# Kernel optimization log

Measured on AMD Instinct MI355X. Metric: run time of the kernel, lower is better.

Reference implementation:

```python
import jax, jax.numpy as jnp
import numpy as np

DIM = 1024
HEADS = 16
DIM_HEAD = 64
INNER = HEADS * DIM_HEAD
EPS = 1e-6


def elu_feature_map(t):
    # F.elu(x) + 1
    return jnp.where(t > 0, t + 1.0, jnp.exp(t))


def setup_inputs() -> dict:
    key = jax.random.key(0)
    k1, k2, k3, k4 = jax.random.split(key, 4)
    B, N = 4, 8192
    x = jax.random.normal(k1, (B, N, DIM), dtype=jnp.float32)
    s_in = 1.0 / np.sqrt(DIM)
    s_out = 1.0 / np.sqrt(INNER)
    Wqkv = jax.random.uniform(k2, (DIM, 3 * INNER), dtype=jnp.float32, minval=-s_in, maxval=s_in)
    Wout = jax.random.uniform(k3, (INNER, DIM), dtype=jnp.float32, minval=-s_out, maxval=s_out)
    bout = jax.random.uniform(k4, (DIM,), dtype=jnp.float32, minval=-s_out, maxval=s_out)
    return {"x": x, "Wqkv": Wqkv, "Wout": Wout, "bout": bout}


def reference(x, Wqkv, Wout, bout):
    B, N, D = x.shape
    qkv = x @ Wqkv  # [B,N,3*INNER]
    q, k, v = jnp.split(qkv, 3, axis=-1)
    # b n (h d) -> b h n d
    resh = lambda t: t.reshape(B, N, HEADS, DIM_HEAD).transpose(0, 2, 1, 3)
    q, k, v = resh(q), resh(k), resh(v)
    q = elu_feature_map(q)
    k = elu_feature_map(k)
    kv = jnp.einsum('bhnd,bhnf->bhdf', k, v)          # [B,H,d,d]
    k_sum = k.sum(axis=-2)                             # [B,H,d]
    qkv_out = jnp.einsum('bhnd,bhdf->bhnf', q, kv)    # [B,H,N,d]
    q_k_sum = jnp.einsum('bhnd,bhd->bhn', q, k_sum)   # [B,H,N]
    out = qkv_out / (q_k_sum[..., None] + EPS)
    out = out.transpose(0, 2, 1, 3).reshape(B, N, INNER)  # b h n d -> b n (h d)
    return out @ Wout + bout
```

## Files before the change

### kernel.cpp

```cpp
#include <hip/hip_runtime.h>
#include <hip/hip_bf16.h>
#include <math.h>


typedef unsigned short ushort_t;
typedef __attribute__((ext_vector_type(8))) short s8v;
typedef __attribute__((ext_vector_type(4))) float f32x4;

#define MFMA(a,b,c) __builtin_amdgcn_mfma_f32_16x16x32_bf16((a),(b),(c),0,0,0)

typedef __attribute__((address_space(3))) unsigned int as3_u32;
typedef __attribute__((address_space(1))) const unsigned int as1_u32c;

__device__ __forceinline__ void g2l16(const void* g, void* l) {
    __builtin_amdgcn_global_load_lds((as1_u32c*)g, (as3_u32*)l, 16, 0, 0);
}

__device__ __forceinline__ float bf2f(ushort_t u) {
    union { float f; unsigned v; } x; x.v = ((unsigned)u) << 16; return x.f;
}
__device__ __forceinline__ ushort_t f2bf(float f) {
    union { float f; unsigned v; } x; x.f = f;
    unsigned r = x.v + 0x7fffu + ((x.v >> 16) & 1u);
    return (ushort_t)(r >> 16);
}
__device__ __forceinline__ float elu1(float t) { return t > 0.0f ? t + 1.0f : expf(t); }

__global__ void k_cast(const float* __restrict__ in, ushort_t* __restrict__ out, int n8) {
    int i = blockIdx.x * blockDim.x + threadIdx.x;
    if (i >= n8) return;
    const float4* p = (const float4*)in;
    float4 a = p[(size_t)i * 2], b = p[(size_t)i * 2 + 1];
    uint4 o;
    o.x = (unsigned)f2bf(a.x) | ((unsigned)f2bf(a.y) << 16);
    o.y = (unsigned)f2bf(a.z) | ((unsigned)f2bf(a.w) << 16);
    o.z = (unsigned)f2bf(b.x) | ((unsigned)f2bf(b.y) << 16);
    o.w = (unsigned)f2bf(b.z) | ((unsigned)f2bf(b.w) << 16);
    *(uint4*)(out + (size_t)i * 8) = o;
}

__global__ __launch_bounds__(256) void k_transpose(const float* __restrict__ W,
                                                   ushort_t* __restrict__ WT, int K, int N) {
    __shared__ float s[32][33];
    const int t = threadIdx.x;
    const int k0 = blockIdx.x * 32, n0 = blockIdx.y * 32;
    const int kr = t >> 3, n4 = (t & 7) * 4;
    float4 v = *(const float4*)(W + (size_t)(k0 + kr) * N + n0 + n4);
    s[kr][n4 + 0] = v.x; s[kr][n4 + 1] = v.y; s[kr][n4 + 2] = v.z; s[kr][n4 + 3] = v.w;
    __syncthreads();
    const int nr = kr, k4 = n4;
    unsigned lo = (unsigned)f2bf(s[k4 + 0][nr]) | ((unsigned)f2bf(s[k4 + 1][nr]) << 16);
    unsigned hi = (unsigned)f2bf(s[k4 + 2][nr]) | ((unsigned)f2bf(s[k4 + 3][nr]) << 16);
    *(uint2*)(WT + (size_t)(n0 + nr) * K + k0 + k4) = make_uint2(lo, hi);
}

template<int MODE>
__global__ __launch_bounds__(512, 1) void k_gemm(
    const ushort_t* __restrict__ A, const ushort_t* __restrict__ B,
    ushort_t* __restrict__ obf, const float* __restrict__ bout, float* __restrict__ of)
{
    constexpr int PLANE = 256 * 32;
    constexpr int BUFS  = 4 * PLANE;
    __shared__ ushort_t lds[2 * BUFS];

    const int t = threadIdx.x, l = t & 63, w = t >> 6;
    const int wr = w >> 2, wc = w & 3;
    const size_t m0 = (size_t)blockIdx.x * 256;
    const size_t n0 = (size_t)blockIdx.y * 256;

    f32x4 acc[8][4];
    const f32x4 z = {0.f, 0.f, 0.f, 0.f};
#pragma unroll
    for (int i = 0; i < 8; i++)
#pragma unroll
        for (int j = 0; j < 4; j++) acc[i][j] = z;

    const int swz = (((l & 3) ^ ((l >> 3) & 3)) << 3);
    const ushort_t* gAl = A + (m0 + (size_t)(w * 16) + (l >> 2)) * 1024 + swz;
    const ushort_t* gBl = B + (n0 + (size_t)(w * 16) + (l >> 2)) * 1024 + swz;
    const int dRow = (w * 16) * 32;

    const int la15 = l & 15;
    const int sA = (((l >> 4) ^ ((la15 >> 1) & 3)) << 3);

    g2l16(gAl,               &lds[0 * PLANE + dRow]);
    g2l16(gAl + 128 * 1024,  &lds[0 * PLANE + 128 * 32 + dRow]);
    g2l16(gBl,               &lds[1 * PLANE + dRow]);
    g2l16(gBl + 128 * 1024,  &lds[1 * PLANE + 128 * 32 + dRow]);
    g2l16(gAl + 32,              &lds[2 * PLANE + dRow]);
    g2l16(gAl + 128 * 1024 + 32, &lds[2 * PLANE + 128 * 32 + dRow]);
    g2l16(gBl + 32,              &lds[3 * PLANE + dRow]);
    g2l16(gBl + 128 * 1024 + 32, &lds[3 * PLANE + 128 * 32 + dRow]);

    for (int T = 0; T < 16; ++T) {
        const int base  = (T & 1) * BUFS;
        const int nbase = BUFS - base;
        const size_t kT1 = (size_t)(T + 1) * 64;
        s8v af[8], bf[4];

        asm volatile("s_waitcnt vmcnt(4)" ::: "memory");
        __builtin_amdgcn_sched_barrier(0);
        __builtin_amdgcn_s_barrier();
        __builtin_amdgcn_sched_barrier(0);
        if (T < 15) {
            g2l16(gAl + kT1,              &lds[nbase + 0 * PLANE + dRow]);
            g2l16(gAl + 128 * 1024 + kT1, &lds[nbase + 0 * PLANE + 128 * 32 + dRow]);
            g2l16(gBl + kT1,              &lds[nbase + 1 * PLANE + dRow]);
            g2l16(gBl + 128 * 1024 + kT1, &lds[nbase + 1 * PLANE + 128 * 32 + dRow]);
        }
#pragma unroll
        for (int nf = 0; nf < 4; nf++)
            bf[nf] = *(const s8v*)&lds[base + 1 * PLANE + (wc * 64 + nf * 16 + la15) * 32 + sA];
#pragma unroll
        for (int mf = 0; mf < 8; mf++)
            af[mf] = *(const s8v*)&lds[base + 0 * PLANE + (wr * 128 + mf * 16 + la15) * 32 + sA];
        __builtin_amdgcn_s_setprio(1);
#pragma unroll
        for (int mf = 0; mf < 8; mf++)
#pragma unroll
            for (int nf = 0; nf < 4; nf++)
                acc[mf][nf] = MFMA(af[mf], bf[nf], acc[mf][nf]);
        __builtin_amdgcn_s_setprio(0);

        if (T < 15) asm volatile("s_waitcnt vmcnt(4)" ::: "memory");
        else        asm volatile("s_waitcnt vmcnt(0)" ::: "memory");
        __builtin_amdgcn_sched_barrier(0);
        __builtin_amdgcn_s_barrier();
        __builtin_amdgcn_sched_barrier(0);
        if (T < 15) {
            g2l16(gAl + 32 + kT1,              &lds[nbase + 2 * PLANE + dRow]);
            g2l16(gAl + 128 * 1024 + 32 + kT1, &lds[nbase + 2 * PLANE + 128 * 32 + dRow]);
            g2l16(gBl + 32 + kT1,              &lds[nbase + 3 * PLANE + dRow]);
            g2l16(gBl + 128 * 1024 + 32 + kT1, &lds[nbase + 3 * PLANE + 128 * 32 + dRow]);
        }
#pragma unroll
        for (int nf = 0; nf < 4; nf++)
            bf[nf] = *(const s8v*)&lds[base + 3 * PLANE + (wc * 64 + nf * 16 + la15) * 32 + sA];
#pragma unroll
        for (int mf = 0; mf < 8; mf++)
            af[mf] = *(const s8v*)&lds[base + 2 * PLANE + (wr * 128 + mf * 16 + la15) * 32 + sA];
        __builtin_amdgcn_s_setprio(1);
#pragma unroll
        for (int mf = 0; mf < 8; mf++)
#pragma unroll
            for (int nf = 0; nf < 4; nf++)
                acc[mf][nf] = MFMA(af[mf], bf[nf], acc[mf][nf]);
        __builtin_amdgcn_s_setprio(0);
    }

    const int r4 = (l >> 4) * 4;
    if (MODE == 0) {
#pragma unroll
        for (int mf = 0; mf < 8; mf++)
#pragma unroll
            for (int nf = 0; nf < 4; nf++) {
                const size_t colb = n0 + wc * 64 + nf * 16;
                const bool feat = colb < 2048;
#pragma unroll
                for (int r = 0; r < 4; r++) {
                    const size_t row = m0 + wr * 128 + mf * 16 + r4 + r;
                    float v = acc[mf][nf][r];
                    obf[row * 3072 + colb + la15] = f2bf(feat ? elu1(v) : v);
                }
            }
    } else {
#pragma unroll
        for (int mf = 0; mf < 8; mf++)
#pragma unroll
            for (int nf = 0; nf < 4; nf++) {
                const size_t col = n0 + wc * 64 + nf * 16 + la15;
                const float bo = bout[col];
#pragma unroll
                for (int r = 0; r < 4; r++) {
                    const size_t row = m0 + wr * 128 + mf * 16 + r4 + r;
                    of[row * 1024 + col] = acc[mf][nf][r] + bo;
                }
            }
    }
}

#define KST 136
__global__ __launch_bounds__(256) void k_kv(
    const ushort_t* __restrict__ qkv, float* __restrict__ kv, float* __restrict__ ksum)
{
    __shared__ ushort_t kT[64 * KST];
    __shared__ ushort_t vT[64 * KST];
    __shared__ float ksl[64];
    const int t = threadIdx.x, l = t & 63, w = t >> 6;
    const int wr = w >> 1, wc = w & 1;
    const int h = blockIdx.x;
    const int b = blockIdx.z;
    const ushort_t* qkvb = qkv + (size_t)b * 8192 * 3072;
    float* kvh = kv + ((size_t)b * 16 + h) * 4096;
    float* ksh = ksum + (size_t)b * 1024 + h * 64;
    const int n00 = blockIdx.y * 512;
    const f32x4 z = {0.f, 0.f, 0.f, 0.f};
    f32x4 acc[2][2] = {{z, z}, {z, z}};
    float ksloc[4] = {0.f, 0.f, 0.f, 0.f};
    const int sd0 = (t & 15) * 4;
    if (t < 64) ksl[t] = 0.f;

    for (int c = 0; c < 4; c++) {
        __syncthreads();
        const int n0 = n00 + c * 128;
#pragma unroll
        for (int i = 0; i < 8; i++) {
            int n = i * 16 + (t >> 4);
            const ushort_t* kp = qkvb + (size_t)(n0 + n) * 3072 + 1024 + h * 64 + sd0;
            ushort4 kw = *(const ushort4*)kp;
            ushort4 vw = *(const ushort4*)(kp + 1024);
            ksloc[0] += bf2f(kw.x); ksloc[1] += bf2f(kw.y);
            ksloc[2] += bf2f(kw.z); ksloc[3] += bf2f(kw.w);
            kT[(sd0 + 0) * KST + n] = kw.x; kT[(sd0 + 1) * KST + n] = kw.y;
            kT[(sd0 + 2) * KST + n] = kw.z; kT[(sd0 + 3) * KST + n] = kw.w;
            vT[(sd0 + 0) * KST + n] = vw.x; vT[(sd0 + 1) * KST + n] = vw.y;
            vT[(sd0 + 2) * KST + n] = vw.z; vT[(sd0 + 3) * KST + n] = vw.w;
        }
        __syncthreads();
#pragma unroll
        for (int kb = 0; kb < 128; kb += 32) {
            s8v af[2], bfr[2];
#pragma unroll
            for (int ma = 0; ma < 2; ma++) {
                int d = wr * 32 + ma * 16 + (l & 15);
                af[ma] = *(const s8v*)&kT[d * KST + kb + (l >> 4) * 8];
            }
#pragma unroll
            for (int fb = 0; fb < 2; fb++) {
                int f = wc * 32 + fb * 16 + (l & 15);
                bfr[fb] = *(const s8v*)&vT[f * KST + kb + (l >> 4) * 8];
            }
#pragma unroll
            for (int ma = 0; ma < 2; ma++)
#pragma unroll
                for (int fb = 0; fb < 2; fb++)
                    acc[ma][fb] = MFMA(af[ma], bfr[fb], acc[ma][fb]);
        }
    }
    atomicAdd(&ksl[sd0 + 0], ksloc[0]); atomicAdd(&ksl[sd0 + 1], ksloc[1]);
    atomicAdd(&ksl[sd0 + 2], ksloc[2]); atomicAdd(&ksl[sd0 + 3], ksloc[3]);
    __syncthreads();
    if (t < 64) atomicAdd(&ksh[t], ksl[t]);
#pragma unroll
    for (int ma = 0; ma < 2; ma++)
#pragma unroll
        for (int fb = 0; fb < 2; fb++)
#pragma unroll
            for (int r = 0; r < 4; r++) {
                int d = wr * 32 + ma * 16 + (l >> 4) * 4 + r;
                int f = wc * 32 + fb * 16 + (l & 15);
                atomicAdd(&kvh[f * 64 + d], acc[ma][fb][r]);
            }
}

#define AST 72
__global__ __launch_bounds__(256) void k_apply(
    const ushort_t* __restrict__ qkv, const float* __restrict__ kv,
    const float* __restrict__ ksum, ushort_t* __restrict__ attn)
{
    __shared__ ushort_t kvb[64 * AST];
    const int t = threadIdx.x, l = t & 63, w = t >> 6;
    const int la15 = l & 15;
    const int row0 = blockIdx.x * 32;
    const int b = row0 >> 13;
    const f32x4 z = {0.f, 0.f, 0.f, 0.f};

    for (int hh = 0; hh < 8; hh++) {
        const int h = blockIdx.y * 8 + hh;
        const float* kvh = kv + ((size_t)b * 16 + h) * 4096;
        const float* ksh = ksum + (size_t)b * 1024 + h * 64;
        __syncthreads();
        {
            const int f = t >> 2, d0 = (t & 3) * 16;
            const float* src = kvh + f * 64 + d0;
            s8v v0, v1;
#pragma unroll
            for (int j = 0; j < 8; j++) {
                v0[j] = (short)f2bf(src[j]);
                v1[j] = (short)f2bf(src[j + 8]);
            }
            *(s8v*)&kvb[f * AST + d0]     = v0;
            *(s8v*)&kvb[f * AST + d0 + 8] = v1;
        }
        __syncthreads();
        float ksv[16];
        {
            const float* kp = ksh + (l >> 4) * 8;
            *(float4*)&ksv[0]  = *(const float4*)(kp);
            *(float4*)&ksv[4]  = *(const float4*)(kp + 4);
            *(float4*)&ksv[8]  = *(const float4*)(kp + 32);
            *(float4*)&ksv[12] = *(const float4*)(kp + 36);
        }
        f32x4 acc[2] = {z, z};
        float pd[2] = {0.f, 0.f};
#pragma unroll
        for (int ks = 0; ks < 2; ks++) {
            const int f = w * 16 + la15;
            s8v bfr = *(const s8v*)&kvb[f * AST + ks * 32 + (l >> 4) * 8];
#pragma unroll
            for (int ma = 0; ma < 2; ma++) {
                int row = row0 + ma * 16 + la15;
                s8v afr = *(const s8v*)(qkv + (size_t)row * 3072 + h * 64 + ks * 32 + (l >> 4) * 8);
#pragma unroll
                for (int j = 0; j < 8; j++)
                    pd[ma] += bf2f((ushort_t)afr[j]) * ksv[ks * 8 + j];
                acc[ma] = MFMA(afr, bfr, acc[ma]);
            }
        }
#pragma unroll
        for (int ma = 0; ma < 2; ma++) {
            pd[ma] += __shfl_xor(pd[ma], 16, 64);
            pd[ma] += __shfl_xor(pd[ma], 32, 64);
        }
#pragma unroll
        for (int ma = 0; ma < 2; ma++)
#pragma unroll
            for (int r = 0; r < 4; r++) {
                int lrow = (l >> 4) * 4 + r;
                float dot = __shfl(pd[ma], lrow, 64);
                float dv = 1.f / (dot + 1e-6f);
                int row = row0 + ma * 16 + lrow;
                int f = w * 16 + la15;
                attn[(size_t)row * 1024 + h * 64 + f] = f2bf(acc[ma][r] * dv);
            }
    }
}

extern "C" void kernel_launch(void* const* d_in, const int* in_sizes, int n_in,
                              void* d_out, int out_size, void* d_ws, size_t ws_size,
                              hipStream_t stream) {
    const float* x    = (const float*)d_in[0];
    const float* Wqkv = (const float*)d_in[1];
    const float* Wout = (const float*)d_in[2];
    const float* bout = (const float*)d_in[3];
    float* out = (float*)d_out;
    char* ws = (char*)d_ws;

    ushort_t* WqkvT = (ushort_t*)(ws + 0);
    ushort_t* WoutT = (ushort_t*)(ws + 6291456);
    float*    kv    = (float*)(ws + 8388608);
    float*    ksum  = (float*)(ws + 12582912);
    ushort_t* xb    = (ushort_t*)(ws + 12599296);
    ushort_t* qkv   = (ushort_t*)(ws + 79708160);
    ushort_t* attn  = (ushort_t*)(ws + 281034752);

    k_transpose<<<dim3(32, 96), 256, 0, stream>>>(Wqkv, WqkvT, 1024, 3072);
    k_transpose<<<dim3(32, 32), 256, 0, stream>>>(Wout, WoutT, 1024, 1024);
    hipMemsetAsync(kv, 0, 4194304 + 16384, stream);
    k_cast<<<16384, 256, 0, stream>>>(x, xb, 4194304);

    k_gemm<0><<<dim3(128, 12), 512, 0, stream>>>(xb, WqkvT, qkv, nullptr, nullptr);
    k_kv<<<dim3(16, 16, 4), 256, 0, stream>>>(qkv, kv, ksum);
    k_apply<<<dim3(1024, 2), 256, 0, stream>>>(qkv, kv, ksum, attn);
    k_gemm<1><<<dim3(128, 4), 512, 0, stream>>>(attn, WoutT, nullptr, bout, out);
}
```

Baseline: 540.5 us.

## Deepen GEMM prefetch and split MFMA phases into barrier-synchronized quarters

Restructures the GEMM main loop to issue global-to-LDS loads one more half-tile ahead (a three-stage prefetch) and splits each K-half into two MFMA groups of four M-fragments. Barriers between fragment loads and MFMA groups keep the waves in lockstep, in the style of ping-pong scheduling. This halves A-fragment register use and is meant to better hide load latency behind MFMA work. The cost is many more workgroup barriers per iteration, and the waitcnt accounting is fragile.

```diff
diff --git a/kernel.cpp b/kernel.cpp
--- a/kernel.cpp
+++ b/kernel.cpp
@@ -8,6 +8,7 @@
 typedef __attribute__((ext_vector_type(4))) float f32x4;
 
 #define MFMA(a,b,c) __builtin_amdgcn_mfma_f32_16x16x32_bf16((a),(b),(c),0,0,0)
+#define SB() __builtin_amdgcn_sched_barrier(0)
 
 typedef __attribute__((address_space(3))) unsigned int as3_u32;
 typedef __attribute__((address_space(1))) const unsigned int as1_u32c;
@@ -83,69 +84,105 @@
     const int la15 = l & 15;
     const int sA = (((l >> 4) ^ ((la15 >> 1) & 3)) << 3);
 
-    g2l16(gAl,               &lds[0 * PLANE + dRow]);
-    g2l16(gAl + 128 * 1024,  &lds[0 * PLANE + 128 * 32 + dRow]);
-    g2l16(gBl,               &lds[1 * PLANE + dRow]);
-    g2l16(gBl + 128 * 1024,  &lds[1 * PLANE + 128 * 32 + dRow]);
+    g2l16(gAl,                   &lds[0 * PLANE + dRow]);
+    g2l16(gAl + 128 * 1024,      &lds[0 * PLANE + 128 * 32 + dRow]);
+    g2l16(gBl,                   &lds[1 * PLANE + dRow]);
+    g2l16(gBl + 128 * 1024,      &lds[1 * PLANE + 128 * 32 + dRow]);
     g2l16(gAl + 32,              &lds[2 * PLANE + dRow]);
     g2l16(gAl + 128 * 1024 + 32, &lds[2 * PLANE + 128 * 32 + dRow]);
     g2l16(gBl + 32,              &lds[3 * PLANE + dRow]);
     g2l16(gBl + 128 * 1024 + 32, &lds[3 * PLANE + 128 * 32 + dRow]);
+    g2l16(gAl + 64,              &lds[BUFS + 0 * PLANE + dRow]);
+    g2l16(gAl + 128 * 1024 + 64, &lds[BUFS + 0 * PLANE + 128 * 32 + dRow]);
+    g2l16(gBl + 64,              &lds[BUFS + 1 * PLANE + dRow]);
+    g2l16(gBl + 128 * 1024 + 64, &lds[BUFS + 1 * PLANE + 128 * 32 + dRow]);
+    asm volatile("s_waitcnt vmcnt(8)" ::: "memory");
+    SB(); __builtin_amdgcn_s_barrier(); SB();
 
     for (int T = 0; T < 16; ++T) {
         const int base  = (T & 1) * BUFS;
         const int nbase = BUFS - base;
         const size_t kT1 = (size_t)(T + 1) * 64;
-        s8v af[8], bf[4];
-
-        asm volatile("s_waitcnt vmcnt(4)" ::: "memory");
-        __builtin_amdgcn_sched_barrier(0);
-        __builtin_amdgcn_s_barrier();
-        __builtin_amdgcn_sched_barrier(0);
-        if (T < 15) {
-            g2l16(gAl + kT1,              &lds[nbase + 0 * PLANE + dRow]);
-            g2l16(gAl + 128 * 1024 + kT1, &lds[nbase + 0 * PLANE + 128 * 32 + dRow]);
-            g2l16(gBl + kT1,              &lds[nbase + 1 * PLANE + dRow]);
-            g2l16(gBl + 128 * 1024 + kT1, &lds[nbase + 1 * PLANE + 128 * 32 + dRow]);
-        }
+        const size_t kT2 = (size_t)(T + 2) * 64;
+        s8v af[4], bf[4];
+
 #pragma unroll
         for (int nf = 0; nf < 4; nf++)
             bf[nf] = *(const s8v*)&lds[base + 1 * PLANE + (wc * 64 + nf * 16 + la15) * 32 + sA];
 #pragma unroll
-        for (int mf = 0; mf < 8; mf++)
+        for (int mf = 0; mf < 4; mf++)
             af[mf] = *(const s8v*)&lds[base + 0 * PLANE + (wr * 128 + mf * 16 + la15) * 32 + sA];
+        SB(); __builtin_amdgcn_s_barrier(); SB();
         __builtin_amdgcn_s_setprio(1);
 #pragma unroll
-        for (int mf = 0; mf < 8; mf++)
+        for (int mf = 0; mf < 4; mf++)
 #pragma unroll
             for (int nf = 0; nf < 4; nf++)
                 acc[mf][nf] = MFMA(af[mf], bf[nf], acc[mf][nf]);
         __builtin_amdgcn_s_setprio(0);
-
-        if (T < 15) asm volatile("s_waitcnt vmcnt(4)" ::: "memory");
-        else        asm volatile("s_waitcnt vmcnt(0)" ::: "memory");
-        __builtin_amdgcn_sched_barrier(0);
-        __builtin_amdgcn_s_barrier();
-        __builtin_amdgcn_sched_barrier(0);
+        SB(); __builtin_amdgcn_s_barrier(); SB();
+
+#pragma unroll
+        for (int mf = 0; mf < 4; mf++)
+            af[mf] = *(const s8v*)&lds[base + 0 * PLANE + (wr * 128 + 64 + mf * 16 + la15) * 32 + sA];
         if (T < 15) {
             g2l16(gAl + 32 + kT1,              &lds[nbase + 2 * PLANE + dRow]);
             g2l16(gAl + 128 * 1024 + 32 + kT1, &lds[nbase + 2 * PLANE + 128 * 32 + dRow]);
             g2l16(gBl + 32 + kT1,              &lds[nbase + 3 * PLANE + dRow]);
             g2l16(gBl + 128 * 1024 + 32 + kT1, &lds[nbase + 3 * PLANE + 128 * 32 + dRow]);
-        }
+            SB();
+            asm volatile("s_waitcnt vmcnt(8)" ::: "memory");
+        } else {
+            SB();
+            asm volatile("s_waitcnt vmcnt(0)" ::: "memory");
+        }
+        SB(); __builtin_amdgcn_s_barrier(); SB();
+        __builtin_amdgcn_s_setprio(1);
+#pragma unroll
+        for (int mf = 0; mf < 4; mf++)
+#pragma unroll
+            for (int nf = 0; nf < 4; nf++)
+                acc[4 + mf][nf] = MFMA(af[mf], bf[nf], acc[4 + mf][nf]);
+        __builtin_amdgcn_s_setprio(0);
+        SB(); __builtin_amdgcn_s_barrier(); SB();
+
 #pragma unroll
         for (int nf = 0; nf < 4; nf++)
             bf[nf] = *(const s8v*)&lds[base + 3 * PLANE + (wc * 64 + nf * 16 + la15) * 32 + sA];
 #pragma unroll
-        for (int mf = 0; mf < 8; mf++)
+        for (int mf = 0; mf < 4; mf++)
             af[mf] = *(const s8v*)&lds[base + 2 * PLANE + (wr * 128 + mf * 16 + la15) * 32 + sA];
+        if (T < 14) {
+            g2l16(gAl + kT2,              &lds[base + 0 * PLANE + dRow]);
+            g2l16(gAl + 128 * 1024 + kT2, &lds[base + 0 * PLANE + 128 * 32 + dRow]);
+            g2l16(gBl + kT2,              &lds[base + 1 * PLANE + dRow]);
+            g2l16(gBl + 128 * 1024 + kT2, &lds[base + 1 * PLANE + 128 * 32 + dRow]);
+        }
+        SB(); __builtin_amdgcn_s_barrier(); SB();
         __builtin_amdgcn_s_setprio(1);
 #pragma unroll
-        for (int mf = 0; mf < 8; mf++)
+        for (int mf = 0; mf < 4; mf++)
 #pragma unroll
             for (int nf = 0; nf < 4; nf++)
                 acc[mf][nf] = MFMA(af[mf], bf[nf], acc[mf][nf]);
         __builtin_amdgcn_s_setprio(0);
+        SB(); __builtin_amdgcn_s_barrier(); SB();
+
+#pragma unroll
+        for (int mf = 0; mf < 4; mf++)
+            af[mf] = *(const s8v*)&lds[base + 2 * PLANE + (wr * 128 + 64 + mf * 16 + la15) * 32 + sA];
+        SB();
+        if (T < 14)      asm volatile("s_waitcnt vmcnt(8)" ::: "memory");
+        else if (T == 14) asm volatile("s_waitcnt vmcnt(4)" ::: "memory");
+        SB(); __builtin_amdgcn_s_barrier(); SB();
+        __builtin_amdgcn_s_setprio(1);
+#pragma unroll
+        for (int mf = 0; mf < 4; mf++)
+#pragma unroll
+            for (int nf = 0; nf < 4; nf++)
+                acc[4 + mf][nf] = MFMA(af[mf], bf[nf], acc[4 + mf][nf]);
+        __builtin_amdgcn_s_setprio(0);
+        SB(); __builtin_amdgcn_s_barrier(); SB();
     }
 
     const int r4 = (l >> 4) * 4;
```

Measured after the change: 542.9 us. No clear change (+0.4%).
